# Kernel tuning notes

Measured on AMD Instinct MI355X. Metric: run time of the kernel, lower is better.

The kernel has to match this reference:

```python
import jax, jax.numpy as jnp
import numpy as np

KH = KW = 3
STRIDE = 1
PAD = 1
DIL = 1


def setup_inputs() -> dict:
    key = jax.random.key(0)
    k1, k2, k3, k4 = jax.random.split(key, 4)
    B, C, H, W = 16, 64, 64, 64
    Cout = 64
    K = KH * KW
    x = jax.random.normal(k1, (B, C, H, W), jnp.float32)
    offset = jax.random.normal(k2, (B, 2 * K, H, W), jnp.float32)
    mask = jax.random.uniform(k3, (B, K, H, W), jnp.float32)
    # uniform(-stdv, stdv) init with stdv = 1/sqrt(C*KH*KW) ~ 0.0417; scaled normal is close enough
    weight = jax.random.normal(k4, (Cout, C, KH, KW), jnp.float32) * 0.04
    bias = jnp.zeros((Cout,), jnp.float32)  # no_bias=True -> frozen zeros, still added
    return dict(input=x, offset=offset, mask=mask, weight=weight, bias=bias)


def _bilinear(img, py, px):
    # img: [C, H, W]; py, px: [K, Ho, Wo] float sampling coords
    # DCNv2 semantics: out-of-bounds corner contributions are zero.
    H, W = img.shape[1], img.shape[2]
    y0f = jnp.floor(py)
    x0f = jnp.floor(px)
    wy = py - y0f
    wx = px - x0f
    y0 = y0f.astype(jnp.int32)
    x0 = x0f.astype(jnp.int32)
    out = jnp.zeros((img.shape[0],) + py.shape, img.dtype)
    for dy in (0, 1):
        for dx in (0, 1):
            yi = y0 + dy
            xi = x0 + dx
            valid = ((yi >= 0) & (yi < H) & (xi >= 0) & (xi < W)).astype(img.dtype)
            v = img[:, jnp.clip(yi, 0, H - 1), jnp.clip(xi, 0, W - 1)]  # [C,K,Ho,Wo]
            w = (wy if dy else 1.0 - wy) * (wx if dx else 1.0 - wx)
            out = out + v * (w * valid)[None]
    return out  # [C, K, Ho, Wo]


def reference(input, offset, mask, weight, bias):
    B, C, H, W = input.shape
    Cout, _, kh, kw = weight.shape
    K = kh * kw
    Ho = (H + 2 * PAD - (DIL * (kh - 1) + 1)) // STRIDE + 1
    Wo = (W + 2 * PAD - (DIL * (kw - 1) + 1)) // STRIDE + 1
    off = offset.reshape(B, K, 2, Ho, Wo)  # per kernel point: (dy, dx)
    ky = jnp.repeat(jnp.arange(kh), kw)  # [K] kernel row index
    kx = jnp.tile(jnp.arange(kw), kh)    # [K] kernel col index
    base_y = jnp.arange(Ho) * STRIDE - PAD
    base_x = jnp.arange(Wo) * STRIDE - PAD
    py = off[:, :, 0] + (base_y[None, None, :, None] + (ky * DIL)[None, :, None, None])
    px = off[:, :, 1] + (base_x[None, None, None, :] + (kx * DIL)[None, :, None, None])
    sampled = jax.vmap(_bilinear)(input, py, px)        # [B, C, K, Ho, Wo]
    modulated = sampled * mask[:, None]                 # mask-modulated accumulation
    out = jnp.einsum('bckpq,ock->bopq', modulated, weight.reshape(Cout, C, K))
    return out + bias[None, :, None, None]
```

## Files before the change

### kernel.cpp

```cpp
#include <hip/hip_runtime.h>
#include <hip/hip_fp16.h>

#define BATCH 16
#define C_IN  64
#define HH    64
#define WW    64
#define COUT  64
#define KK    9
#define HW    4096
#define CK    576
#define WROWS 13
#define WLO   5

typedef _Float16 f16x8 __attribute__((ext_vector_type(8)));
typedef float    f32x4 __attribute__((ext_vector_type(4)));

__device__ __forceinline__ unsigned short f32_to_f16u(float f) {
    _Float16 h = (_Float16)f;
    unsigned short u;
    __builtin_memcpy(&u, &h, 2);
    return u;
}

__device__ __forceinline__ __half2 as_h2(unsigned int u) {
    __half2 r; __builtin_memcpy(&r, &u, 4); return r;
}
__device__ __forceinline__ unsigned int as_u32(__half2 v) {
    unsigned int u; __builtin_memcpy(&u, &v, 4); return u;
}

__global__ __launch_bounds__(256) void prep_kernel(
    const float* __restrict__ x, const float* __restrict__ w,
    unsigned short* __restrict__ xt, unsigned short* __restrict__ wt) {
    __shared__ unsigned short tile[64][72];
    const int t = threadIdx.x;
    const int blk = blockIdx.x;
    if (blk < 1024) {
        const int b = blk >> 6, y = blk & 63;
        const float* xrow = x + ((b * 64) * 64 + y) * 64;
#pragma unroll
        for (int it = 0; it < 4; ++it) {
            const int idx = it * 256 + t;
            const int c = idx >> 4, seg = idx & 15;
            const float4 v = *(const float4*)(xrow + c * HW + seg * 4);
            tile[seg * 4 + 0][c] = f32_to_f16u(v.x);
            tile[seg * 4 + 1][c] = f32_to_f16u(v.y);
            tile[seg * 4 + 2][c] = f32_to_f16u(v.z);
            tile[seg * 4 + 3][c] = f32_to_f16u(v.w);
        }
        __syncthreads();
#pragma unroll
        for (int it = 0; it < 2; ++it) {
            const int idx = it * 256 + t;
            const int xx = idx >> 3, cs = idx & 7;
            *(int4*)&xt[((b * HW) + y * 64 + xx) * 64 + cs * 8] =
                *(const int4*)&tile[xx][cs * 8];
        }
    } else {
        const int i = (blk - 1024) * 256 + t;
        const int j = i & 7;
        const int l = (i >> 3) & 63;
        const int ot = (i >> 9) & 3;
        const int r = i >> 11;
        const int ks = r % 6, kc = r / 6;
        const int o  = ot * 16 + (l & 15);
        const int kk = ks * 32 + (l >> 4) * 8 + j;
        const int tap = kk >> 6, c = kk & 63;
        const int k = kc * 3 + tap;
        wt[i] = f32_to_f16u(w[o * CK + c * KK + k]);
    }
}

__global__ __launch_bounds__(512, 1) void dcn_main_kernel(
    const float* __restrict__ offset, const float* __restrict__ mask,
    const unsigned short* __restrict__ xt, const unsigned short* __restrict__ wt,
    const float* __restrict__ bias, float* __restrict__ out) {
    __shared__ __align__(16) unsigned short win[WROWS * 4096];
    __shared__ __align__(16) int PWw[2][576 * 4];
    __shared__ __align__(16) unsigned int PWa[2][576 * 4];

    const int t    = threadIdx.x;
    const int wave = __builtin_amdgcn_readfirstlane(t >> 6);
    const int lane = t & 63;
    const int quad = lane >> 4, m16 = lane & 15;
    const int rw   = wave >> 2;
    const int qb   = (wave & 3) * 16;

    const int blk = blockIdx.x;
    const int xcd = blk & 7;
    const int i6  = blk >> 3;
    const int b   = (xcd << 1) | (i6 >> 5);
    const int R   = (i6 & 31) * 2;
    const int base = R - WLO;

    const float* offb = offset + b * (2 * KK * HW);
    const float* mb   = mask + b * (KK * HW);
    const char* xtb   = (const char*)(xt + b * (HW * 64));

    float oyv[3], oxv[3], mkv[3];
#pragma unroll
    for (int p = 0; p < 3; ++p) {
        const int it = p * 512 + t;
        if (it < 1152) {
            const int rsel = it >= 576;
            const int j = it - rsel * 576;
            const int tap = j >> 6, q = j & 63;
            const int rowX = R + rsel;
            oyv[p] = offb[(2 * tap) * HW + rowX * 64 + q];
            oxv[p] = offb[(2 * tap + 1) * HW + rowX * 64 + q];
            mkv[p] = mb[tap * HW + rowX * 64 + q];
        } else { oyv[p] = 0.f; oxv[p] = 0.f; mkv[p] = 0.f; }
    }
    asm volatile("" :: "v"(oyv[0]), "v"(oxv[0]), "v"(mkv[0]),
                       "v"(oyv[1]), "v"(oxv[1]), "v"(mkv[1]),
                       "v"(oyv[2]), "v"(oxv[2]), "v"(mkv[2]));

    const int pxl = t >> 3;
    const int swb = ((t & 7) ^ (pxl & 7)) << 4;
#pragma unroll
    for (int s = 0; s < WROWS; ++s) {
        const int srcrow = min(max(base + s, 0), HH - 1);
        const char* src = xtb + srcrow * 8192 + pxl * 128 + swb;
        __builtin_amdgcn_global_load_lds(
            (const __attribute__((address_space(1))) unsigned int*)src,
            (__attribute__((address_space(3))) unsigned int*)
                ((char*)win + s * 8192 + t * 16),
            16, 0, 0);
    }
    __builtin_amdgcn_sched_barrier(0);

#pragma unroll
    for (int p = 0; p < 3; ++p) {
        const int it = p * 512 + t;
        if (it < 1152) {
            const int rsel = it >= 576;
            const int j = it - rsel * 576;
            const int tap = j >> 6, q = j & 63;
            const int rowX = R + rsel;
            const int ky = (tap * 11) >> 5;
            const int kx = tap - ky * 3;
            const float py  = oyv[p] + (float)(rowX - 1 + ky);
            const float pxf = oxv[p] + (float)(q - 1 + kx);
            const float y0f = floorf(py), x0f = floorf(pxf);
            const float wy = py - y0f, wx = pxf - x0f;
            const int y0 = (int)y0f, x0 = (int)x0f;
            const int y1 = y0 + 1,   x1 = x0 + 1;
            const float vy0 = (y0 >= 0 && y0 < HH) ? 1.f : 0.f;
            const float vy1 = (y1 >= 0 && y1 < HH) ? 1.f : 0.f;
            const float vx0 = (x0 >= 0 && x0 < WW) ? 1.f : 0.f;
            const float vx1 = (x1 >= 0 && x1 < WW) ? 1.f : 0.f;
            const float mk = mkv[p];
            const float w00 = (1.f - wy) * (1.f - wx) * vy0 * vx0 * mk;
            const float w01 = (1.f - wy) * wx         * vy0 * vx1 * mk;
            const float w10 = wy * (1.f - wx)         * vy1 * vx0 * mk;
            const float w11 = wy * wx                 * vy1 * vx1 * mk;
            const int cy0 = min(max(y0, 0), HH - 1), cy1 = min(max(y1, 0), HH - 1);
            const int cx0 = min(max(x0, 0), WW - 1), cx1 = min(max(x1, 0), WW - 1);
            const int sl0 = cy0 - base, sl1 = cy1 - base;
            const unsigned esc = (sl0 < 0) | (sl1 > (WROWS - 1));
            const int c0 = min(max(sl0, 0), WROWS - 1);
            const int c1 = min(max(sl1, 0), WROWS - 1);
            const int wl00 = c0 * 64 + cx0, wl01 = c0 * 64 + cx1;
            const int wl10 = c1 * 64 + cx0, wl11 = c1 * 64 + cx1;
            const unsigned int s00 = f32_to_f16u(w00);
            const unsigned int s01 = f32_to_f16u(w01);
            const unsigned int s10 = f32_to_f16u(w10);
            const unsigned int s11 = f32_to_f16u(w11);
            int4 P0;
            P0.x = (int)(s00 | (s00 << 16));
            P0.y = (int)(s01 | (s01 << 16));
            P0.z = (int)(s10 | (s10 << 16));
            P0.w = (int)(s11 | (s11 << 16));
            *(int4*)&PWw[rsel][j * 4] = P0;
            uint4 A;
            A.x = (unsigned)((wl00 << 7) | ((wl00 & 7) << 4)) | (esc << 31);
            A.y = (unsigned)((wl01 << 7) | ((wl01 & 7) << 4));
            A.z = (unsigned)((wl10 << 7) | ((wl10 & 7) << 4));
            A.w = (unsigned)((wl11 << 7) | ((wl11 & 7) << 4));
            *(uint4*)&PWa[rsel][j * 4] = A;
        }
    }
    __syncthreads();

    f32x4 acc[4];
#pragma unroll
    for (int ot = 0; ot < 4; ++ot)
#pragma unroll
        for (int r = 0; r < 4; ++r) acc[ot][r] = 0.f;

    const char* winc = (const char*)win;
    const int rowX = R + rw;

#pragma unroll
    for (int kc = 0; kc < 3; ++kc) {
        const unsigned short* wkc = wt + kc * (6 * 4 * 512);

        uint4 A3[3];
        int4  P3[3];
#pragma unroll
        for (int tp = 0; tp < 3; ++tp) {
            const int it = (kc * 3 + tp) * 64 + qb + m16;
            A3[tp] = *(const uint4*)&PWa[rw][it * 4];
            P3[tp] = *(const int4*)&PWw[rw][it * 4];
        }

        uint4 qv[6][4];
#pragma unroll
        for (int ks = 0; ks < 6; ++ks) {
            const int tp = ks >> 1;
            const unsigned sswz = (unsigned)(((ks & 1) * 4 + quad) << 4);
            qv[ks][0] = *(const uint4*)(winc + ((A3[tp].x & 0x7FFFFFFFu) ^ sswz));
            qv[ks][1] = *(const uint4*)(winc + (A3[tp].y ^ sswz));
            qv[ks][2] = *(const uint4*)(winc + (A3[tp].z ^ sswz));
            qv[ks][3] = *(const uint4*)(winc + (A3[tp].w ^ sswz));
        }

        const int anyesc = (int)(A3[0].x >> 31) | (int)(A3[1].x >> 31) |
                           (int)(A3[2].x >> 31);
        if (__builtin_expect(__any(anyesc), 0)) {
#pragma unroll
            for (int ks = 0; ks < 6; ++ks) {
                const int tp = ks >> 1;
                if (A3[tp].x >> 31) {
                    const int tap = kc * 3 + tp;
                    const int qq = qb + m16;
                    const int ky = (tap * 11) >> 5;
                    const int kx = tap - ky * 3;
                    const float oy = offb[(2 * tap) * HW + rowX * 64 + qq];
                    const float ox = offb[(2 * tap + 1) * HW + rowX * 64 + qq];
                    const float py  = oy + (float)(rowX - 1 + ky);
                    const float pxf = ox + (float)(qq - 1 + kx);
                    const int y0 = (int)floorf(py), x0 = (int)floorf(pxf);
                    const int cy0 = min(max(y0, 0), HH - 1);
                    const int cy1 = min(max(y0 + 1, 0), HH - 1);
                    const int cx0 = min(max(x0, 0), WW - 1);
                    const int cx1 = min(max(x0 + 1, 0), WW - 1);
                    const int hoff = (ks & 1) * 64 + quad * 16;
                    qv[ks][0] = *(const uint4*)(xtb + ((cy0 * 64 + cx0) << 7) + hoff);
                    qv[ks][1] = *(const uint4*)(xtb + ((cy0 * 64 + cx1) << 7) + hoff);
                    qv[ks][2] = *(const uint4*)(xtb + ((cy1 * 64 + cx0) << 7) + hoff);
                    qv[ks][3] = *(const uint4*)(xtb + ((cy1 * 64 + cx1) << 7) + hoff);
                }
            }
        }

#pragma unroll
        for (int ks = 0; ks < 6; ++ks) {
            const int4 p0 = P3[ks >> 1];
            const __half2 c00 = as_h2((unsigned)p0.x);
            const __half2 c01 = as_h2((unsigned)p0.y);
            const __half2 c10 = as_h2((unsigned)p0.z);
            const __half2 c11 = as_h2((unsigned)p0.w);
            const uint4 q0 = qv[ks][0], q1 = qv[ks][1];
            const uint4 q2 = qv[ks][2], q3 = qv[ks][3];
            uint4 ov;
            {
                __half2 v = __hmul2(c00, as_h2(q0.x));
                v = __hfma2(c01, as_h2(q1.x), v);
                v = __hfma2(c10, as_h2(q2.x), v);
                v = __hfma2(c11, as_h2(q3.x), v);
                ov.x = as_u32(v);
            }
            {
                __half2 v = __hmul2(c00, as_h2(q0.y));
                v = __hfma2(c01, as_h2(q1.y), v);
                v = __hfma2(c10, as_h2(q2.y), v);
                v = __hfma2(c11, as_h2(q3.y), v);
                ov.y = as_u32(v);
            }
            {
                __half2 v = __hmul2(c00, as_h2(q0.z));
                v = __hfma2(c01, as_h2(q1.z), v);
                v = __hfma2(c10, as_h2(q2.z), v);
                v = __hfma2(c11, as_h2(q3.z), v);
                ov.z = as_u32(v);
            }
            {
                __half2 v = __hmul2(c00, as_h2(q0.w));
                v = __hfma2(c01, as_h2(q1.w), v);
                v = __hfma2(c10, as_h2(q2.w), v);
                v = __hfma2(c11, as_h2(q3.w), v);
                ov.w = as_u32(v);
            }
            f16x8 bfrag;
            __builtin_memcpy(&bfrag, &ov, 16);
#pragma unroll
            for (int ot = 0; ot < 4; ++ot) {
                const f16x8 afrag =
                    *(const f16x8*)(wkc + (ks * 4 + ot) * 512 + lane * 8);
                acc[ot] = __builtin_amdgcn_mfma_f32_16x16x32_f16(afrag, bfrag,
                                                                 acc[ot], 0, 0, 0);
            }
        }
    }

    float* ob = out + b * (COUT * HW) + rowX * 64 + qb + m16;
#pragma unroll
    for (int ot = 0; ot < 4; ++ot)
#pragma unroll
        for (int r = 0; r < 4; ++r) {
            const int o = ot * 16 + quad * 4 + r;
            ob[o * HW] = acc[ot][r] + bias[o];
        }
}

extern "C" void kernel_launch(void* const* d_in, const int* in_sizes, int n_in,
                              void* d_out, int out_size, void* d_ws,
                              size_t ws_size, hipStream_t stream) {
    const float* x    = (const float*)d_in[0];
    const float* off  = (const float*)d_in[1];
    const float* mask = (const float*)d_in[2];
    const float* w    = (const float*)d_in[3];
    const float* bias = (const float*)d_in[4];
    float* out = (float*)d_out;

    unsigned short* xt = (unsigned short*)d_ws;
    unsigned short* wt = (unsigned short*)((char*)d_ws + 8388608);

    prep_kernel<<<1024 + 144, 256, 0, stream>>>(x, w, xt, wt);
    dcn_main_kernel<<<512, 512, 0, stream>>>(off, mask, xt, wt, bias, out);
}
```

Baseline: 98.82 us.

## Process four output rows per block with a taller LDS window and packed tables

Each block now covers four output rows instead of two, using a 15-row LDS window of the input and looping twice over row pairs. This halves the grid to 256 blocks and amortises the input-window load across more rows. The per-sample bilinear weights and LDS addresses are packed as 16-bit values in uint2 entries to keep LDS use within budget, with the weights expanded back into half2 at use. The trade-off is fewer blocks than there are CUs (256 on MI355X), a longer serial loop per block, and extra unpack ALU work.

```diff
diff --git a/kernel.cpp b/kernel.cpp
--- a/kernel.cpp
+++ b/kernel.cpp
@@ -9,7 +9,7 @@
 #define KK    9
 #define HW    4096
 #define CK    576
-#define WROWS 13
+#define WROWS 15
 #define WLO   5
 
 typedef _Float16 f16x8 __attribute__((ext_vector_type(8)));
@@ -76,8 +76,8 @@
     const unsigned short* __restrict__ xt, const unsigned short* __restrict__ wt,
     const float* __restrict__ bias, float* __restrict__ out) {
     __shared__ __align__(16) unsigned short win[WROWS * 4096];
-    __shared__ __align__(16) int PWw[2][576 * 4];
-    __shared__ __align__(16) unsigned int PWa[2][576 * 4];
+    __shared__ __align__(8) uint2 PWw[4][576];
+    __shared__ __align__(8) uint2 PWa[4][576];
 
     const int t    = threadIdx.x;
     const int wave = __builtin_amdgcn_readfirstlane(t >> 6);
@@ -88,24 +88,22 @@
 
     const int blk = blockIdx.x;
     const int xcd = blk & 7;
-    const int i6  = blk >> 3;
-    const int b   = (xcd << 1) | (i6 >> 5);
-    const int R   = (i6 & 31) * 2;
-    const int base = R - WLO;
+    const int i5  = blk >> 3;
+    const int b   = (xcd << 1) | (i5 >> 4);
+    const int R4  = (i5 & 15) * 4;
+    const int base = R4 - WLO;
 
     const float* offb = offset + b * (2 * KK * HW);
     const float* mb   = mask + b * (KK * HW);
     const char* xtb   = (const char*)(xt + b * (HW * 64));
 
-    float oyv[3], oxv[3], mkv[3];
-#pragma unroll
-    for (int p = 0; p < 3; ++p) {
+    float oyv[5], oxv[5], mkv[5];
+#pragma unroll
+    for (int p = 0; p < 5; ++p) {
         const int it = p * 512 + t;
-        if (it < 1152) {
-            const int rsel = it >= 576;
-            const int j = it - rsel * 576;
-            const int tap = j >> 6, q = j & 63;
-            const int rowX = R + rsel;
+        if (it < 2304) {
+            const int tap = it >> 8, rowi = (it >> 6) & 3, q = it & 63;
+            const int rowX = R4 + rowi;
             oyv[p] = offb[(2 * tap) * HW + rowX * 64 + q];
             oxv[p] = offb[(2 * tap + 1) * HW + rowX * 64 + q];
             mkv[p] = mb[tap * HW + rowX * 64 + q];
@@ -114,6 +112,8 @@
     asm volatile("" :: "v"(oyv[0]), "v"(oxv[0]), "v"(mkv[0]),
                        "v"(oyv[1]), "v"(oxv[1]), "v"(mkv[1]),
                        "v"(oyv[2]), "v"(oxv[2]), "v"(mkv[2]));
+    asm volatile("" :: "v"(oyv[3]), "v"(oxv[3]), "v"(mkv[3]),
+                       "v"(oyv[4]), "v"(oxv[4]), "v"(mkv[4]));
 
     const int pxl = t >> 3;
     const int swb = ((t & 7) ^ (pxl & 7)) << 4;
@@ -130,13 +130,11 @@
     __builtin_amdgcn_sched_barrier(0);
 
 #pragma unroll
-    for (int p = 0; p < 3; ++p) {
+    for (int p = 0; p < 5; ++p) {
         const int it = p * 512 + t;
-        if (it < 1152) {
-            const int rsel = it >= 576;
-            const int j = it - rsel * 576;
-            const int tap = j >> 6, q = j & 63;
-            const int rowX = R + rsel;
+        if (it < 2304) {
+            const int tap = it >> 8, rowi = (it >> 6) & 3, q = it & 63;
+            const int rowX = R4 + rowi;
             const int ky = (tap * 11) >> 5;
             const int kx = tap - ky * 3;
             const float py  = oyv[p] + (float)(rowX - 1 + ky);
@@ -162,146 +160,154 @@
             const int c1 = min(max(sl1, 0), WROWS - 1);
             const int wl00 = c0 * 64 + cx0, wl01 = c0 * 64 + cx1;
             const int wl10 = c1 * 64 + cx0, wl11 = c1 * 64 + cx1;
-            const unsigned int s00 = f32_to_f16u(w00);
-            const unsigned int s01 = f32_to_f16u(w01);
-            const unsigned int s10 = f32_to_f16u(w10);
-            const unsigned int s11 = f32_to_f16u(w11);
-            int4 P0;
-            P0.x = (int)(s00 | (s00 << 16));
-            P0.y = (int)(s01 | (s01 << 16));
-            P0.z = (int)(s10 | (s10 << 16));
-            P0.w = (int)(s11 | (s11 << 16));
-            *(int4*)&PWw[rsel][j * 4] = P0;
-            uint4 A;
-            A.x = (unsigned)((wl00 << 7) | ((wl00 & 7) << 4)) | (esc << 31);
-            A.y = (unsigned)((wl01 << 7) | ((wl01 & 7) << 4));
-            A.z = (unsigned)((wl10 << 7) | ((wl10 & 7) << 4));
-            A.w = (unsigned)((wl11 << 7) | ((wl11 & 7) << 4));
-            *(uint4*)&PWa[rsel][j * 4] = A;
+            const unsigned e00 = (unsigned)((wl00 << 3) | (wl00 & 7)) | (esc << 15);
+            const unsigned e01 = (unsigned)((wl01 << 3) | (wl01 & 7));
+            const unsigned e10 = (unsigned)((wl10 << 3) | (wl10 & 7));
+            const unsigned e11 = (unsigned)((wl11 << 3) | (wl11 & 7));
+            const unsigned s00 = f32_to_f16u(w00);
+            const unsigned s01 = f32_to_f16u(w01);
+            const unsigned s10 = f32_to_f16u(w10);
+            const unsigned s11 = f32_to_f16u(w11);
+            uint2 Wp; Wp.x = s00 | (s01 << 16); Wp.y = s10 | (s11 << 16);
+            uint2 Aa; Aa.x = e00 | (e01 << 16); Aa.y = e10 | (e11 << 16);
+            PWw[rowi][tap * 64 + q] = Wp;
+            PWa[rowi][tap * 64 + q] = Aa;
         }
     }
     __syncthreads();
 
-    f32x4 acc[4];
-#pragma unroll
-    for (int ot = 0; ot < 4; ++ot)
-#pragma unroll
-        for (int r = 0; r < 4; ++r) acc[ot][r] = 0.f;
-
     const char* winc = (const char*)win;
-    const int rowX = R + rw;
-
-#pragma unroll
-    for (int kc = 0; kc < 3; ++kc) {
-        const unsigned short* wkc = wt + kc * (6 * 4 * 512);
-
-        uint4 A3[3];
-        int4  P3[3];
-#pragma unroll
-        for (int tp = 0; tp < 3; ++tp) {
-            const int it = (kc * 3 + tp) * 64 + qb + m16;
-            A3[tp] = *(const uint4*)&PWa[rw][it * 4];
-            P3[tp] = *(const int4*)&PWw[rw][it * 4];
-        }
-
-        uint4 qv[6][4];
-#pragma unroll
-        for (int ks = 0; ks < 6; ++ks) {
-            const int tp = ks >> 1;
-            const unsigned sswz = (unsigned)(((ks & 1) * 4 + quad) << 4);
-            qv[ks][0] = *(const uint4*)(winc + ((A3[tp].x & 0x7FFFFFFFu) ^ sswz));
-            qv[ks][1] = *(const uint4*)(winc + (A3[tp].y ^ sswz));
-            qv[ks][2] = *(const uint4*)(winc + (A3[tp].z ^ sswz));
-            qv[ks][3] = *(const uint4*)(winc + (A3[tp].w ^ sswz));
-        }
-
-        const int anyesc = (int)(A3[0].x >> 31) | (int)(A3[1].x >> 31) |
-                           (int)(A3[2].x >> 31);
-        if (__builtin_expect(__any(anyesc), 0)) {
+
+#pragma unroll 1
+    for (int pr = 0; pr < 2; ++pr) {
+        f32x4 acc[4];
+#pragma unroll
+        for (int ot = 0; ot < 4; ++ot)
+#pragma unroll
+            for (int r = 0; r < 4; ++r) acc[ot][r] = 0.f;
+
+        const int arow = pr * 2 + rw;
+        const int rowX = R4 + arow;
+
+#pragma unroll
+        for (int kc = 0; kc < 3; ++kc) {
+            const unsigned short* wkc = wt + kc * (6 * 4 * 512);
+
+            uint2 A3[3], W3[3];
+#pragma unroll
+            for (int tp = 0; tp < 3; ++tp) {
+                const int it = (kc * 3 + tp) * 64 + qb + m16;
+                A3[tp] = PWa[arow][it];
+                W3[tp] = PWw[arow][it];
+            }
+
+            uint4 qv[6][4];
 #pragma unroll
             for (int ks = 0; ks < 6; ++ks) {
                 const int tp = ks >> 1;
-                if (A3[tp].x >> 31) {
-                    const int tap = kc * 3 + tp;
-                    const int qq = qb + m16;
-                    const int ky = (tap * 11) >> 5;
-                    const int kx = tap - ky * 3;
-                    const float oy = offb[(2 * tap) * HW + rowX * 64 + qq];
-                    const float ox = offb[(2 * tap + 1) * HW + rowX * 64 + qq];
-                    const float py  = oy + (float)(rowX - 1 + ky);
-                    const float pxf = ox + (float)(qq - 1 + kx);
-                    const int y0 = (int)floorf(py), x0 = (int)floorf(pxf);
-                    const int cy0 = min(max(y0, 0), HH - 1);
-                    const int cy1 = min(max(y0 + 1, 0), HH - 1);
-                    const int cx0 = min(max(x0, 0), WW - 1);
-                    const int cx1 = min(max(x0 + 1, 0), WW - 1);
-                    const int hoff = (ks & 1) * 64 + quad * 16;
-                    qv[ks][0] = *(const uint4*)(xtb + ((cy0 * 64 + cx0) << 7) + hoff);
-                    qv[ks][1] = *(const uint4*)(xtb + ((cy0 * 64 + cx1) << 7) + hoff);
-                    qv[ks][2] = *(const uint4*)(xtb + ((cy1 * 64 + cx0) << 7) + hoff);
-                    qv[ks][3] = *(const uint4*)(xtb + ((cy1 * 64 + cx1) << 7) + hoff);
+                const unsigned sswz = (unsigned)(((ks & 1) * 4 + quad) << 4);
+                const unsigned e00 = A3[tp].x & 0x7FFFu;
+                const unsigned e01 = A3[tp].x >> 16;
+                const unsigned e10 = A3[tp].y & 0xFFFFu;
+                const unsigned e11 = A3[tp].y >> 16;
+                qv[ks][0] = *(const uint4*)(winc + ((e00 << 4) ^ sswz));
+                qv[ks][1] = *(const uint4*)(winc + ((e01 << 4) ^ sswz));
+                qv[ks][2] = *(const uint4*)(winc + ((e10 << 4) ^ sswz));
+                qv[ks][3] = *(const uint4*)(winc + ((e11 << 4) ^ sswz));
+            }
+
+            const int anyesc =
+                (int)(((A3[0].x | A3[1].x | A3[2].x) >> 15) & 1u);
+            if (__builtin_expect(__any(anyesc), 0)) {
+#pragma unroll
+                for (int ks = 0; ks < 6; ++ks) {
+                    const int tp = ks >> 1;
+                    if ((A3[tp].x >> 15) & 1u) {
+                        const int tap = kc * 3 + tp;
+                        const int qq = qb + m16;
+                        const int ky = (tap * 11) >> 5;
+                        const int kx = tap - ky * 3;
+                        const float oy = offb[(2 * tap) * HW + rowX * 64 + qq];
+                        const float ox = offb[(2 * tap + 1) * HW + rowX * 64 + qq];
+                        const float py  = oy + (float)(rowX - 1 + ky);
+                        const float pxf = ox + (float)(qq - 1 + kx);
+                        const int y0 = (int)floorf(py), x0 = (int)floorf(pxf);
+                        const int cy0 = min(max(y0, 0), HH - 1);
+                        const int cy1 = min(max(y0 + 1, 0), HH - 1);
+                        const int cx0 = min(max(x0, 0), WW - 1);
+                        const int cx1 = min(max(x0 + 1, 0), WW - 1);
+                        const int hoff = (ks & 1) * 64 + quad * 16;
+                        qv[ks][0] = *(const uint4*)(xtb + ((cy0 * 64 + cx0) << 7) + hoff);
+                        qv[ks][1] = *(const uint4*)(xtb + ((cy0 * 64 + cx1) << 7) + hoff);
+                        qv[ks][2] = *(const uint4*)(xtb + ((cy1 * 64 + cx0) << 7) + hoff);
+                        qv[ks][3] = *(const uint4*)(xtb + ((cy1 * 64 + cx1) << 7) + hoff);
+                    }
+                }
+            }
+
+#pragma unroll
+            for (int ks = 0; ks < 6; ++ks) {
+                const uint2 Wp = W3[ks >> 1];
+                unsigned ulo = Wp.x & 0xFFFFu;
+                const __half2 c00 = as_h2(ulo | (ulo << 16));
+                unsigned uhi = Wp.x >> 16;
+                const __half2 c01 = as_h2(uhi | (uhi << 16));
+                unsigned vlo = Wp.y & 0xFFFFu;
+                const __half2 c10 = as_h2(vlo | (vlo << 16));
+                unsigned vhi = Wp.y >> 16;
+                const __half2 c11 = as_h2(vhi | (vhi << 16));
+                const uint4 q0 = qv[ks][0], q1 = qv[ks][1];
+                const uint4 q2 = qv[ks][2], q3 = qv[ks][3];
+                uint4 ov;
+                {
+                    __half2 v = __hmul2(c00, as_h2(q0.x));
+                    v = __hfma2(c01, as_h2(q1.x), v);
+                    v = __hfma2(c10, as_h2(q2.x), v);
+                    v = __hfma2(c11, as_h2(q3.x), v);
+                    ov.x = as_u32(v);
+                }
+                {
+                    __half2 v = __hmul2(c00, as_h2(q0.y));
+                    v = __hfma2(c01, as_h2(q1.y), v);
+                    v = __hfma2(c10, as_h2(q2.y), v);
+                    v = __hfma2(c11, as_h2(q3.y), v);
+                    ov.y = as_u32(v);
+                }
+                {
+                    __half2 v = __hmul2(c00, as_h2(q0.z));
+                    v = __hfma2(c01, as_h2(q1.z), v);
+                    v = __hfma2(c10, as_h2(q2.z), v);
+                    v = __hfma2(c11, as_h2(q3.z), v);
+                    ov.z = as_u32(v);
+                }
+                {
+                    __half2 v = __hmul2(c00, as_h2(q0.w));
+                    v = __hfma2(c01, as_h2(q1.w), v);
+                    v = __hfma2(c10, as_h2(q2.w), v);
+                    v = __hfma2(c11, as_h2(q3.w), v);
+                    ov.w = as_u32(v);
+                }
+                f16x8 bfrag;
+                __builtin_memcpy(&bfrag, &ov, 16);
+#pragma unroll
+                for (int ot = 0; ot < 4; ++ot) {
+                    const f16x8 afrag =
+                        *(const f16x8*)(wkc + (ks * 4 + ot) * 512 + lane * 8);
+                    acc[ot] = __builtin_amdgcn_mfma_f32_16x16x32_f16(
+                        afrag, bfrag, acc[ot], 0, 0, 0);
                 }
             }
         }
 
-#pragma unroll
-        for (int ks = 0; ks < 6; ++ks) {
-            const int4 p0 = P3[ks >> 1];
-            const __half2 c00 = as_h2((unsigned)p0.x);
-            const __half2 c01 = as_h2((unsigned)p0.y);
-            const __half2 c10 = as_h2((unsigned)p0.z);
-            const __half2 c11 = as_h2((unsigned)p0.w);
-            const uint4 q0 = qv[ks][0], q1 = qv[ks][1];
-            const uint4 q2 = qv[ks][2], q3 = qv[ks][3];
-            uint4 ov;
-            {
-                __half2 v = __hmul2(c00, as_h2(q0.x));
-                v = __hfma2(c01, as_h2(q1.x), v);
-                v = __hfma2(c10, as_h2(q2.x), v);
-                v = __hfma2(c11, as_h2(q3.x), v);
-                ov.x = as_u32(v);
-            }
-            {
-                __half2 v = __hmul2(c00, as_h2(q0.y));
-                v = __hfma2(c01, as_h2(q1.y), v);
-                v = __hfma2(c10, as_h2(q2.y), v);
-                v = __hfma2(c11, as_h2(q3.y), v);
-                ov.y = as_u32(v);
-            }
-            {
-                __half2 v = __hmul2(c00, as_h2(q0.z));
-                v = __hfma2(c01, as_h2(q1.z), v);
-                v = __hfma2(c10, as_h2(q2.z), v);
-                v = __hfma2(c11, as_h2(q3.z), v);
-                ov.z = as_u32(v);
-            }
-            {
-                __half2 v = __hmul2(c00, as_h2(q0.w));
-                v = __hfma2(c01, as_h2(q1.w), v);
-                v = __hfma2(c10, as_h2(q2.w), v);
-                v = __hfma2(c11, as_h2(q3.w), v);
-                ov.w = as_u32(v);
-            }
-            f16x8 bfrag;
-            __builtin_memcpy(&bfrag, &ov, 16);
-#pragma unroll
-            for (int ot = 0; ot < 4; ++ot) {
-                const f16x8 afrag =
-                    *(const f16x8*)(wkc + (ks * 4 + ot) * 512 + lane * 8);
-                acc[ot] = __builtin_amdgcn_mfma_f32_16x16x32_f16(afrag, bfrag,
-                                                                 acc[ot], 0, 0, 0);
-            }
-        }
-    }
-
-    float* ob = out + b * (COUT * HW) + rowX * 64 + qb + m16;
-#pragma unroll
-    for (int ot = 0; ot < 4; ++ot)
-#pragma unroll
-        for (int r = 0; r < 4; ++r) {
-            const int o = ot * 16 + quad * 4 + r;
-            ob[o * HW] = acc[ot][r] + bias[o];
-        }
+        float* ob = out + b * (COUT * HW) + rowX * 64 + qb + m16;
+#pragma unroll
+        for (int ot = 0; ot < 4; ++ot)
+#pragma unroll
+            for (int r = 0; r < 4; ++r) {
+                const int o = ot * 16 + quad * 4 + r;
+                ob[o * HW] = acc[ot][r] + bias[o];
+            }
+    }
 }
 
 extern "C" void kernel_launch(void* const* d_in, const int* in_sizes, int n_in,
@@ -318,5 +324,5 @@
     unsigned short* wt = (unsigned short*)((char*)d_ws + 8388608);
 
     prep_kernel<<<1024 + 144, 256, 0, stream>>>(x, w, xt, wt);
-    dcn_main_kernel<<<512, 512, 0, stream>>>(off, mask, xt, wt, bias, out);
-}
+    dcn_main_kernel<<<256, 512, 0, stream>>>(off, mask, xt, wt, bias, out);
+}
```

New measurement: 176.1 us. 1.78x slower.
